# Kernel tuning notes

Hardware: AMD Instinct MI355X
Metric: run time of the kernel (lower is better)

## Reference

```python
import jax, jax.numpy as jnp
import numpy as np

N_NODES = 50000
N_EDGES = 800000
NUM_GRAPHS = 4
IN_DIM, HID_DIM, OUT_DIM = 1024, 128, 1
MAX_RISK = 5.0


def gcn_conv(x, W, b, src, dst, n):
    """PyG GCNConv: add self-loops, sym-normalize, gather-GEMM-scatter."""
    loop = jnp.arange(n, dtype=src.dtype)
    s = jnp.concatenate([src, loop])
    d = jnp.concatenate([dst, loop])
    deg = jax.ops.segment_sum(jnp.ones_like(d, dtype=x.dtype), d, num_segments=n)
    dinv = jnp.where(deg > 0, jax.lax.rsqrt(deg), 0.0)
    norm = dinv[s] * dinv[d]  # [E+N]
    xw = x @ W                # dense GEMM first (fewer FLOPs than per-edge)
    msg = xw[s] * norm[:, None]          # irregular gather, [E+N, out]
    out = jax.ops.segment_sum(msg, d, num_segments=n)  # scatter-add
    return out + b


def setup_inputs() -> dict:
    key = jax.random.key(0)
    ks = jax.random.split(key, 12)
    x = jax.random.normal(ks[0], (N_NODES, IN_DIM), dtype=jnp.float32)
    edge_index = jax.random.randint(ks[1], (2, N_EDGES), 0, N_NODES, dtype=jnp.int64)
    batch = jnp.sort(jax.random.randint(ks[2], (N_NODES,), 0, NUM_GRAPHS, dtype=jnp.int64))

    def glorot(k, fan_in, fan_out):
        s = np.sqrt(6.0 / (fan_in + fan_out)).astype(np.float32)
        return jax.random.uniform(k, (fan_in, fan_out), jnp.float32, -s, s)

    params = {
        'W0': glorot(ks[3], IN_DIM, HID_DIM),  'b0': jnp.zeros((HID_DIM,), jnp.float32),
        'W1': glorot(ks[4], HID_DIM, HID_DIM), 'b1': jnp.zeros((HID_DIM,), jnp.float32),
        'W2': glorot(ks[5], HID_DIM, HID_DIM), 'b2': jnp.zeros((HID_DIM,), jnp.float32),
        'Wl1': glorot(ks[6], 2 * HID_DIM, HID_DIM), 'bl1': jnp.zeros((HID_DIM,), jnp.float32),
        'Wl2': glorot(ks[7], HID_DIM, HID_DIM // 2), 'bl2': jnp.zeros((HID_DIM // 2,), jnp.float32),
        'Wl3': glorot(ks[8], HID_DIM // 2, OUT_DIM), 'bl3': jnp.zeros((OUT_DIM,), jnp.float32),
    }
    return dict(x=x, edge_index=edge_index, batch=batch, **params)


def reference(x, edge_index, batch, W0, b0, W1, b1, W2, b2, Wl1, bl1, Wl2, bl2, Wl3, bl3):
    n = x.shape[0]
    src, dst = edge_index[0], edge_index[1]
    h = jax.nn.relu(gcn_conv(x, W0, b0, src, dst, n))
    h = jax.nn.relu(gcn_conv(h, W1, b1, src, dst, n))
    h = jax.nn.relu(gcn_conv(h, W2, b2, src, dst, n))
    # global max pool + global mean pool per graph
    gmax = jax.ops.segment_max(h, batch, num_segments=NUM_GRAPHS)
    gsum = jax.ops.segment_sum(h, batch, num_segments=NUM_GRAPHS)
    cnt = jax.ops.segment_sum(jnp.ones((n,), h.dtype), batch, num_segments=NUM_GRAPHS)
    gmean = gsum / jnp.maximum(cnt, 1.0)[:, None]
    g = jnp.concatenate([gmax, gmean], axis=1)  # [G, 2*hid]
    g = jax.nn.relu(g @ Wl1 + bl1)
    g = jax.nn.relu(g @ Wl2 + bl2)
    out = g @ Wl3 + bl3
    return jnp.minimum(out, MAX_RISK)
```

## Files before the change

kernel.cpp:

```cpp
#include <hip/hip_runtime.h>
#include <math.h>

#define HID 128
#define NGRAPH 4

typedef int idx_t;
typedef short bf16x8 __attribute__((ext_vector_type(8)));
typedef float f32x4 __attribute__((ext_vector_type(4)));
typedef _Float16 f16x8 __attribute__((ext_vector_type(8)));

__device__ inline ushort f2bf(float f) {
  uint u = __float_as_uint(f);
  u += 0x7FFF + ((u >> 16) & 1);
  return (ushort)(u >> 16);
}
__device__ inline float bf2f(ushort h) { return __uint_as_float(((uint)h) << 16); }

__device__ inline int sw(int row, int slot) {
  return (row << 5) + ((slot ^ ((row >> 1) & 3)) << 3);
}

__global__ __launch_bounds__(256) void k_count(const idx_t* __restrict__ dst,
                                               int* __restrict__ cnt, int E) {
  int e = blockIdx.x * 256 + threadIdx.x;
  if (e < E) atomicAdd(&cnt[dst[e]], 1);
}

#define SC 1024
__global__ __launch_bounds__(256) void k_scan1(const int* __restrict__ cnt,
                                               int* __restrict__ bsum, int n) {
  __shared__ int sh[256];
  int base = blockIdx.x * SC + threadIdx.x * 4;
  int s = 0;
#pragma unroll
  for (int j = 0; j < 4; ++j) { int i = base + j; if (i < n) s += cnt[i]; }
  sh[threadIdx.x] = s;
  __syncthreads();
  for (int o = 128; o > 0; o >>= 1) {
    if (threadIdx.x < o) sh[threadIdx.x] += sh[threadIdx.x + o];
    __syncthreads();
  }
  if (threadIdx.x == 0) bsum[blockIdx.x] = sh[0];
}

__global__ __launch_bounds__(64) void k_scan2(const int* __restrict__ bsum,
                                              int* __restrict__ boff,
                                              int* __restrict__ off, int nb, int n) {
  int lane = threadIdx.x;
  int v = (lane < nb) ? bsum[lane] : 0;
  for (int d = 1; d < 64; d <<= 1) {
    int t = __shfl_up(v, d);
    if (lane >= d) v += t;
  }
  int ex = __shfl_up(v, 1);
  if (lane == 0) ex = 0;
  if (lane < nb) boff[lane] = ex;
  if (lane == nb - 1) off[n] = v;
}

__global__ __launch_bounds__(256) void k_scan3(const int* __restrict__ cnt,
                                               const int* __restrict__ boff,
                                               int* __restrict__ off,
                                               float* __restrict__ dinv, int n) {
  __shared__ int sh[256];
  int base = blockIdx.x * SC + threadIdx.x * 4;
  int c[4];
  int s = 0;
#pragma unroll
  for (int j = 0; j < 4; ++j) {
    int i = base + j;
    c[j] = (i < n) ? cnt[i] : 0;
    s += c[j];
  }
  sh[threadIdx.x] = s;
  __syncthreads();
  for (int o = 1; o < 256; o <<= 1) {
    int t = (threadIdx.x >= (unsigned)o) ? sh[threadIdx.x - o] : 0;
    __syncthreads();
    sh[threadIdx.x] += t;
    __syncthreads();
  }
  int ex = sh[threadIdx.x] - s + boff[blockIdx.x];
#pragma unroll
  for (int j = 0; j < 4; ++j) {
    int i = base + j;
    if (i < n) {
      off[i] = ex;
      dinv[i] = 1.0f / sqrtf((float)c[j] + 1.0f);
      ex += c[j];
    }
  }
}

__global__ __launch_bounds__(256) void k_fill(const idx_t* __restrict__ src,
                                              const idx_t* __restrict__ dst,
                                              const int* __restrict__ off,
                                              const float* __restrict__ dinv,
                                              int* __restrict__ fillc,
                                              int2* __restrict__ edata, int E) {
  int e = blockIdx.x * 256 + threadIdx.x;
  if (e < E) {
    int s = src[e], d = dst[e];
    int p = atomicAdd(&fillc[d], 1);
    float w = dinv[s] * dinv[d];
    edata[off[d] + p] = make_int2(s, __float_as_int(w));
  }
}

__global__ __launch_bounds__(256) void k_wsplit(const float* __restrict__ W,
                                                ushort* __restrict__ Wh,
                                                ushort* __restrict__ Wl, int K) {
  int i = blockIdx.x * 256 + threadIdx.x;
  if (i >= K * HID) return;
  int k = i >> 7, n = i & 127;
  float f = W[i];
  ushort h = f2bf(f);
  Wh[(size_t)n * K + k] = h;
  Wl[(size_t)n * K + k] = f2bf(f - bf2f(h));
}

template <int K>
__global__ __launch_bounds__(256) void k_gemm_mfma(const float* __restrict__ X,
                                                   const ushort* __restrict__ Wh,
                                                   const ushort* __restrict__ Wl,
                                                   float* __restrict__ Y,
                                                   _Float16* __restrict__ Y16,
                                                   int M) {
  __shared__ __align__(16) ushort Ah[128 * 32];
  __shared__ __align__(16) ushort Al[128 * 32];
  __shared__ __align__(16) ushort Bh[128 * 32];
  __shared__ __align__(16) ushort Bl[128 * 32];
  int tid = threadIdx.x;
  int wid = tid >> 6, lane = tid & 63;
  int lrow = lane & 15, kg = lane >> 4;
  int row0 = blockIdx.x * 128;
  f32x4 acc[2][8] = {};

  for (int k0 = 0; k0 < K; k0 += 32) {
#pragma unroll
    for (int p = 0; p < 2; ++p) {
      int g = tid + (p << 8);
      int r = g >> 2, s = g & 3;
      int grow = row0 + r;
      float xv[8] = {0.f, 0.f, 0.f, 0.f, 0.f, 0.f, 0.f, 0.f};
      if (grow < M) {
        const float4 v0 = *(const float4*)&X[(size_t)grow * K + k0 + s * 8];
        const float4 v1 = *(const float4*)&X[(size_t)grow * K + k0 + s * 8 + 4];
        xv[0] = v0.x; xv[1] = v0.y; xv[2] = v0.z; xv[3] = v0.w;
        xv[4] = v1.x; xv[5] = v1.y; xv[6] = v1.z; xv[7] = v1.w;
      }
      bf16x8 hv, lv;
#pragma unroll
      for (int j = 0; j < 8; ++j) {
        ushort hb = f2bf(xv[j]);
        hv[j] = (short)hb;
        lv[j] = (short)f2bf(xv[j] - bf2f(hb));
      }
      *(bf16x8*)&Ah[sw(r, s)] = hv;
      *(bf16x8*)&Al[sw(r, s)] = lv;
    }
#pragma unroll
    for (int p = 0; p < 2; ++p) {
      int g = tid + (p << 8);
      int c = g >> 2, s = g & 3;
      *(bf16x8*)&Bh[sw(c, s)] = *(const bf16x8*)&Wh[(size_t)c * K + k0 + s * 8];
      *(bf16x8*)&Bl[sw(c, s)] = *(const bf16x8*)&Wl[(size_t)c * K + k0 + s * 8];
    }
    __syncthreads();

    bf16x8 ah[2], al[2];
#pragma unroll
    for (int mi = 0; mi < 2; ++mi) {
      int r = wid * 32 + mi * 16 + lrow;
      ah[mi] = *(const bf16x8*)&Ah[sw(r, kg)];
      al[mi] = *(const bf16x8*)&Al[sw(r, kg)];
    }
#pragma unroll
    for (int ni = 0; ni < 8; ++ni) {
      int c = ni * 16 + lrow;
      bf16x8 bh = *(const bf16x8*)&Bh[sw(c, kg)];
      bf16x8 bl = *(const bf16x8*)&Bl[sw(c, kg)];
#pragma unroll
      for (int mi = 0; mi < 2; ++mi) {
        acc[mi][ni] = __builtin_amdgcn_mfma_f32_16x16x32_bf16(ah[mi], bh, acc[mi][ni], 0, 0, 0);
        acc[mi][ni] = __builtin_amdgcn_mfma_f32_16x16x32_bf16(al[mi], bh, acc[mi][ni], 0, 0, 0);
        acc[mi][ni] = __builtin_amdgcn_mfma_f32_16x16x32_bf16(ah[mi], bl, acc[mi][ni], 0, 0, 0);
      }
    }
    __syncthreads();
  }
#pragma unroll
  for (int mi = 0; mi < 2; ++mi)
#pragma unroll
    for (int ni = 0; ni < 8; ++ni)
#pragma unroll
      for (int r = 0; r < 4; ++r) {
        int grow = row0 + wid * 32 + mi * 16 + kg * 4 + r;
        if (grow < M) {
          float val = acc[mi][ni][r];
          Y[(size_t)grow * HID + ni * 16 + lrow] = val;
          Y16[(size_t)grow * HID + ni * 16 + lrow] = (_Float16)val;
        }
      }
}

__global__ __launch_bounds__(256) void k_agg16(const float* __restrict__ xw,
                                               const _Float16* __restrict__ xh,
                                               const float* __restrict__ dinv,
                                               const int* __restrict__ off,
                                               const int2* __restrict__ edata,
                                               const float* __restrict__ bias,
                                               float* __restrict__ hout, int n) {
  int v = blockIdx.x * 4 + (threadIdx.x >> 6);
  if (v >= n) return;
  int lane = threadIdx.x & 63;
  int grp = lane >> 4, gl = lane & 15;
  int fb = gl * 8;
  float acc[8] = {0.f, 0.f, 0.f, 0.f, 0.f, 0.f, 0.f, 0.f};
  int j0 = off[v], j1 = off[v + 1];
  for (int j = j0 + grp; j < j1; j += 4) {
    int2 e = edata[j];
    float w = __int_as_float(e.y);
    f16x8 m = *(const f16x8*)&xh[(size_t)e.x * HID + fb];
#pragma unroll
    for (int q = 0; q < 8; ++q) acc[q] = fmaf(w, (float)m[q], acc[q]);
  }
#pragma unroll
  for (int q = 0; q < 8; ++q) {
    acc[q] += __shfl_xor(acc[q], 16);
    acc[q] += __shfl_xor(acc[q], 32);
  }
  if (grp == 0) {
    float dv = dinv[v], dv2 = dv * dv;
    const float4 s0 = *(const float4*)&xw[(size_t)v * HID + fb];
    const float4 s1 = *(const float4*)&xw[(size_t)v * HID + fb + 4];
    const float4 b0 = *(const float4*)&bias[fb];
    const float4 b1 = *(const float4*)&bias[fb + 4];
    float4 o0, o1;
    o0.x = fmaxf(fmaf(dv2, s0.x, acc[0]) + b0.x, 0.f);
    o0.y = fmaxf(fmaf(dv2, s0.y, acc[1]) + b0.y, 0.f);
    o0.z = fmaxf(fmaf(dv2, s0.z, acc[2]) + b0.z, 0.f);
    o0.w = fmaxf(fmaf(dv2, s0.w, acc[3]) + b0.w, 0.f);
    o1.x = fmaxf(fmaf(dv2, s1.x, acc[4]) + b1.x, 0.f);
    o1.y = fmaxf(fmaf(dv2, s1.y, acc[5]) + b1.y, 0.f);
    o1.z = fmaxf(fmaf(dv2, s1.z, acc[6]) + b1.z, 0.f);
    o1.w = fmaxf(fmaf(dv2, s1.w, acc[7]) + b1.w, 0.f);
    *(float4*)&hout[(size_t)v * HID + fb] = o0;
    *(float4*)&hout[(size_t)v * HID + fb + 4] = o1;
  }
}

__global__ __launch_bounds__(256) void k_gcnt(const idx_t* __restrict__ batch,
                                              int* __restrict__ gcnt, int n) {
  __shared__ int h[NGRAPH];
  int tid = threadIdx.x;
  if (tid < NGRAPH) h[tid] = 0;
  __syncthreads();
  int i = blockIdx.x * 256 + tid;
  if (i < n) atomicAdd(&h[batch[i]], 1);
  __syncthreads();
  if (tid < NGRAPH && h[tid]) atomicAdd(&gcnt[tid], h[tid]);
}

__global__ __launch_bounds__(128) void k_pool(const float* __restrict__ h,
                                              const idx_t* __restrict__ batch,
                                              float* __restrict__ gmax,
                                              float* __restrict__ gsum, int n) {
  int f = threadIdx.x;
  int v0 = blockIdx.x * 128;
  int cur = -1;
  float mx = 0.f, sm = 0.f;
  for (int i = 0; i < 128; ++i) {
    int v = v0 + i;
    if (v >= n) break;
    int g = batch[v];
    if (g != cur) {
      if (cur >= 0) {
        atomicMax((int*)&gmax[cur * HID + f], __float_as_int(mx));
        atomicAdd(&gsum[cur * HID + f], sm);
      }
      cur = g; mx = 0.f; sm = 0.f;
    }
    float val = h[(size_t)v * HID + f];
    mx = fmaxf(mx, val);
    sm += val;
  }
  if (cur >= 0) {
    atomicMax((int*)&gmax[cur * HID + f], __float_as_int(mx));
    atomicAdd(&gsum[cur * HID + f], sm);
  }
}

__global__ __launch_bounds__(256) void k_mlp(const float* __restrict__ gmax,
                                             const float* __restrict__ gsum,
                                             const int* __restrict__ gcnt,
                                             const float* __restrict__ Wl1,
                                             const float* __restrict__ bl1,
                                             const float* __restrict__ Wl2,
                                             const float* __restrict__ bl2,
                                             const float* __restrict__ Wl3,
                                             const float* __restrict__ bl3,
                                             float* __restrict__ out) {
  __shared__ float G[NGRAPH][2 * HID];
  __shared__ float H1[NGRAPH][HID];
  __shared__ float H2[NGRAPH][HID / 2];
  int t = threadIdx.x;
  for (int i = t; i < NGRAPH * 2 * HID; i += 256) {
    int gi = i >> 8, j = i & 255;
    float val;
    if (j < HID) val = gmax[gi * HID + j];
    else val = gsum[gi * HID + (j - HID)] / fmaxf((float)gcnt[gi], 1.0f);
    G[gi][j] = val;
  }
  __syncthreads();
  for (int i = t; i < NGRAPH * HID; i += 256) {
    int gi = i >> 7, j = i & 127;
    float a = bl1[j];
    for (int k = 0; k < 2 * HID; ++k) a = fmaf(G[gi][k], Wl1[k * HID + j], a);
    H1[gi][j] = fmaxf(a, 0.f);
  }
  __syncthreads();
  {
    int gi = t >> 6, j = t & 63;
    float a = bl2[j];
    for (int k = 0; k < HID; ++k) a = fmaf(H1[gi][k], Wl2[k * 64 + j], a);
    H2[gi][j] = fmaxf(a, 0.f);
  }
  __syncthreads();
  if (t < NGRAPH) {
    float a = bl3[0];
    for (int k = 0; k < 64; ++k) a = fmaf(H2[t][k], Wl3[k], a);
    out[t] = fminf(a, 5.0f);
  }
}

extern "C" void kernel_launch(void* const* d_in, const int* in_sizes, int n_in,
                              void* d_out, int out_size, void* d_ws, size_t ws_size,
                              hipStream_t stream) {
  const float* x   = (const float*)d_in[0];
  const idx_t* ei  = (const idx_t*)d_in[1];
  const idx_t* bat = (const idx_t*)d_in[2];
  const float* W0 = (const float*)d_in[3];  const float* b0 = (const float*)d_in[4];
  const float* W1 = (const float*)d_in[5];  const float* b1 = (const float*)d_in[6];
  const float* W2 = (const float*)d_in[7];  const float* b2 = (const float*)d_in[8];
  const float* Wl1 = (const float*)d_in[9];  const float* bl1 = (const float*)d_in[10];
  const float* Wl2 = (const float*)d_in[11]; const float* bl2 = (const float*)d_in[12];
  const float* Wl3 = (const float*)d_in[13]; const float* bl3 = (const float*)d_in[14];
  float* out = (float*)d_out;

  const int N = in_sizes[2];
  const int E = in_sizes[1] / 2;
  const idx_t* srcv = ei;
  const idx_t* dstv = ei + E;
  const int nb = (N + SC - 1) / SC;

  char* ws = (char*)d_ws;
  size_t o = 0;
  auto alloc = [&](size_t bytes) -> void* {
    void* p = ws + o;
    o = (o + bytes + 255) & ~(size_t)255;
    return p;
  };
  float* bufA      = (float*)alloc((size_t)N * HID * 4);
  _Float16* bufA16 = (_Float16*)alloc((size_t)N * HID * 2);
  float* bufB      = (float*)alloc((size_t)N * HID * 4);
  float* dinv = (float*)alloc((size_t)N * 4);
  int* cnt    = (int*)alloc((size_t)N * 4);
  int* off    = (int*)alloc((size_t)(N + 1) * 4);
  int* fillc  = (int*)alloc((size_t)N * 4);
  int2* edata = (int2*)alloc((size_t)E * 8);
  int* bsum   = (int*)alloc(64 * 4);
  int* boff   = (int*)alloc(64 * 4);
  ushort* Wh0 = (ushort*)alloc((size_t)1024 * HID * 2);
  ushort* Wl0 = (ushort*)alloc((size_t)1024 * HID * 2);
  ushort* Wh1 = (ushort*)alloc((size_t)HID * HID * 2);
  ushort* Wlo1 = (ushort*)alloc((size_t)HID * HID * 2);
  ushort* Wh2 = (ushort*)alloc((size_t)HID * HID * 2);
  ushort* Wlo2 = (ushort*)alloc((size_t)HID * HID * 2);
  float* gmax = (float*)alloc(NGRAPH * HID * 4);
  float* gsum = (float*)alloc(NGRAPH * HID * 4);
  int* gcnt   = (int*)alloc(NGRAPH * 4);

  hipMemsetAsync(cnt, 0, (size_t)N * 4, stream);
  hipMemsetAsync(fillc, 0, (size_t)N * 4, stream);
  hipMemsetAsync(gmax, 0, NGRAPH * HID * 4, stream);
  hipMemsetAsync(gsum, 0, NGRAPH * HID * 4, stream);
  hipMemsetAsync(gcnt, 0, NGRAPH * 4, stream);

  k_wsplit<<<(1024 * HID + 255) / 256, 256, 0, stream>>>(W0, Wh0, Wl0, 1024);
  k_wsplit<<<(HID * HID + 255) / 256, 256, 0, stream>>>(W1, Wh1, Wlo1, HID);
  k_wsplit<<<(HID * HID + 255) / 256, 256, 0, stream>>>(W2, Wh2, Wlo2, HID);

  k_count<<<(E + 255) / 256, 256, 0, stream>>>(dstv, cnt, E);
  k_scan1<<<nb, 256, 0, stream>>>(cnt, bsum, N);
  k_scan2<<<1, 64, 0, stream>>>(bsum, boff, off, nb, N);
  k_scan3<<<nb, 256, 0, stream>>>(cnt, boff, off, dinv, N);
  k_fill<<<(E + 255) / 256, 256, 0, stream>>>(srcv, dstv, off, dinv, fillc, edata, E);

  const int gblk = (N + 127) / 128;
  const int ablk = (N + 3) / 4;
  k_gemm_mfma<1024><<<gblk, 256, 0, stream>>>(x, Wh0, Wl0, bufA, bufA16, N);
  k_agg16<<<ablk, 256, 0, stream>>>(bufA, bufA16, dinv, off, edata, b0, bufB, N);
  k_gemm_mfma<HID><<<gblk, 256, 0, stream>>>(bufB, Wh1, Wlo1, bufA, bufA16, N);
  k_agg16<<<ablk, 256, 0, stream>>>(bufA, bufA16, dinv, off, edata, b1, bufB, N);
  k_gemm_mfma<HID><<<gblk, 256, 0, stream>>>(bufB, Wh2, Wlo2, bufA, bufA16, N);
  k_agg16<<<ablk, 256, 0, stream>>>(bufA, bufA16, dinv, off, edata, b2, bufB, N);

  k_gcnt<<<(N + 255) / 256, 256, 0, stream>>>(bat, gcnt, N);
  k_pool<<<(N + 127) / 128, 128, 0, stream>>>(bufB, bat, gmax, gsum, N);
  k_mlp<<<1, 256, 0, stream>>>(gmax, gsum, gcnt, Wl1, bl1, Wl2, bl2, Wl3, bl3, out);
}
```

Measured before the change: 410.0 us.

## Split-K the first GEMM and drop the fp32 GEMM output copy

The 1024-wide first-layer GEMM is split four ways along K across a second grid dimension. Each split writes fp32 partials, and a new reduction kernel sums them into fp16. This gives 1564 blocks instead of 391 to fill the GPU's CUs. The GEMMs also stop writing the fp32 copy, and aggregation reads its self-loop term from the fp16 buffer, which removes a store and a read of N*128 floats per layer. In exchange, split-K adds 4x N*128 fp32 partial writes plus a reduction pass, and the self-loop term loses precision.

```diff
diff --git a/kernel.cpp b/kernel.cpp
--- a/kernel.cpp
+++ b/kernel.cpp
@@ -119,11 +119,11 @@
   Wl[(size_t)n * K + k] = f2bf(f - bf2f(h));
 }
 
-template <int K>
+template <int K, int KS>
 __global__ __launch_bounds__(256) void k_gemm_mfma(const float* __restrict__ X,
                                                    const ushort* __restrict__ Wh,
                                                    const ushort* __restrict__ Wl,
-                                                   float* __restrict__ Y,
+                                                   float* __restrict__ Ypart,
                                                    _Float16* __restrict__ Y16,
                                                    int M) {
   __shared__ __align__(16) ushort Ah[128 * 32];
@@ -134,9 +134,11 @@
   int wid = tid >> 6, lane = tid & 63;
   int lrow = lane & 15, kg = lane >> 4;
   int row0 = blockIdx.x * 128;
+  constexpr int KC = K / KS;
+  int kbase = (KS > 1) ? blockIdx.y * KC : 0;
   f32x4 acc[2][8] = {};
 
-  for (int k0 = 0; k0 < K; k0 += 32) {
+  for (int k0 = kbase; k0 < kbase + KC; k0 += 32) {
 #pragma unroll
     for (int p = 0; p < 2; ++p) {
       int g = tid + (p << 8);
@@ -189,23 +191,49 @@
     }
     __syncthreads();
   }
-#pragma unroll
-  for (int mi = 0; mi < 2; ++mi)
-#pragma unroll
-    for (int ni = 0; ni < 8; ++ni)
-#pragma unroll
-      for (int r = 0; r < 4; ++r) {
-        int grow = row0 + wid * 32 + mi * 16 + kg * 4 + r;
-        if (grow < M) {
-          float val = acc[mi][ni][r];
-          Y[(size_t)grow * HID + ni * 16 + lrow] = val;
-          Y16[(size_t)grow * HID + ni * 16 + lrow] = (_Float16)val;
+  if (KS > 1) {
+    float* yp = Ypart + (size_t)blockIdx.y * M * HID;
+#pragma unroll
+    for (int mi = 0; mi < 2; ++mi)
+#pragma unroll
+      for (int ni = 0; ni < 8; ++ni)
+#pragma unroll
+        for (int r = 0; r < 4; ++r) {
+          int grow = row0 + wid * 32 + mi * 16 + kg * 4 + r;
+          if (grow < M) yp[(size_t)grow * HID + ni * 16 + lrow] = acc[mi][ni][r];
         }
-      }
-}
-
-__global__ __launch_bounds__(256) void k_agg16(const float* __restrict__ xw,
-                                               const _Float16* __restrict__ xh,
+  } else {
+#pragma unroll
+    for (int mi = 0; mi < 2; ++mi)
+#pragma unroll
+      for (int ni = 0; ni < 8; ++ni)
+#pragma unroll
+        for (int r = 0; r < 4; ++r) {
+          int grow = row0 + wid * 32 + mi * 16 + kg * 4 + r;
+          if (grow < M)
+            Y16[(size_t)grow * HID + ni * 16 + lrow] = (_Float16)acc[mi][ni][r];
+        }
+  }
+}
+
+__global__ __launch_bounds__(256) void k_red(const float* __restrict__ part,
+                                             _Float16* __restrict__ o16,
+                                             size_t total) {
+  size_t i = ((size_t)blockIdx.x * 256 + threadIdx.x) * 4;
+  if (i >= total) return;
+  float4 a = *(const float4*)&part[i];
+  float4 b = *(const float4*)&part[i + total];
+  float4 c = *(const float4*)&part[i + 2 * total];
+  float4 d = *(const float4*)&part[i + 3 * total];
+  _Float16 r[4];
+  r[0] = (_Float16)(a.x + b.x + c.x + d.x);
+  r[1] = (_Float16)(a.y + b.y + c.y + d.y);
+  r[2] = (_Float16)(a.z + b.z + c.z + d.z);
+  r[3] = (_Float16)(a.w + b.w + c.w + d.w);
+  *(short4*)&o16[i] = *(short4*)r;
+}
+
+__global__ __launch_bounds__(256) void k_agg16(const _Float16* __restrict__ xh,
                                                const float* __restrict__ dinv,
                                                const int* __restrict__ off,
                                                const int2* __restrict__ edata,
@@ -232,19 +260,18 @@
   }
   if (grp == 0) {
     float dv = dinv[v], dv2 = dv * dv;
-    const float4 s0 = *(const float4*)&xw[(size_t)v * HID + fb];
-    const float4 s1 = *(const float4*)&xw[(size_t)v * HID + fb + 4];
+    f16x8 sv = *(const f16x8*)&xh[(size_t)v * HID + fb];
     const float4 b0 = *(const float4*)&bias[fb];
     const float4 b1 = *(const float4*)&bias[fb + 4];
     float4 o0, o1;
-    o0.x = fmaxf(fmaf(dv2, s0.x, acc[0]) + b0.x, 0.f);
-    o0.y = fmaxf(fmaf(dv2, s0.y, acc[1]) + b0.y, 0.f);
-    o0.z = fmaxf(fmaf(dv2, s0.z, acc[2]) + b0.z, 0.f);
-    o0.w = fmaxf(fmaf(dv2, s0.w, acc[3]) + b0.w, 0.f);
-    o1.x = fmaxf(fmaf(dv2, s1.x, acc[4]) + b1.x, 0.f);
-    o1.y = fmaxf(fmaf(dv2, s1.y, acc[5]) + b1.y, 0.f);
-    o1.z = fmaxf(fmaf(dv2, s1.z, acc[6]) + b1.z, 0.f);
-    o1.w = fmaxf(fmaf(dv2, s1.w, acc[7]) + b1.w, 0.f);
+    o0.x = fmaxf(fmaf(dv2, (float)sv[0], acc[0]) + b0.x, 0.f);
+    o0.y = fmaxf(fmaf(dv2, (float)sv[1], acc[1]) + b0.y, 0.f);
+    o0.z = fmaxf(fmaf(dv2, (float)sv[2], acc[2]) + b0.z, 0.f);
+    o0.w = fmaxf(fmaf(dv2, (float)sv[3], acc[3]) + b0.w, 0.f);
+    o1.x = fmaxf(fmaf(dv2, (float)sv[4], acc[4]) + b1.x, 0.f);
+    o1.y = fmaxf(fmaf(dv2, (float)sv[5], acc[5]) + b1.y, 0.f);
+    o1.z = fmaxf(fmaf(dv2, (float)sv[6], acc[6]) + b1.z, 0.f);
+    o1.w = fmaxf(fmaf(dv2, (float)sv[7], acc[7]) + b1.w, 0.f);
     *(float4*)&hout[(size_t)v * HID + fb] = o0;
     *(float4*)&hout[(size_t)v * HID + fb + 4] = o1;
   }
@@ -361,9 +388,9 @@
     o = (o + bytes + 255) & ~(size_t)255;
     return p;
   };
-  float* bufA      = (float*)alloc((size_t)N * HID * 4);
-  _Float16* bufA16 = (_Float16*)alloc((size_t)N * HID * 2);
-  float* bufB      = (float*)alloc((size_t)N * HID * 4);
+  _Float16* xh   = (_Float16*)alloc((size_t)N * HID * 2);
+  float* bufB    = (float*)alloc((size_t)N * HID * 4);
+  float* part    = (float*)alloc((size_t)4 * N * HID * 4);
   float* dinv = (float*)alloc((size_t)N * 4);
   int* cnt    = (int*)alloc((size_t)N * 4);
   int* off    = (int*)alloc((size_t)(N + 1) * 4);
@@ -399,12 +426,14 @@
 
   const int gblk = (N + 127) / 128;
   const int ablk = (N + 3) / 4;
-  k_gemm_mfma<1024><<<gblk, 256, 0, stream>>>(x, Wh0, Wl0, bufA, bufA16, N);
-  k_agg16<<<ablk, 256, 0, stream>>>(bufA, bufA16, dinv, off, edata, b0, bufB, N);
-  k_gemm_mfma<HID><<<gblk, 256, 0, stream>>>(bufB, Wh1, Wlo1, bufA, bufA16, N);
-  k_agg16<<<ablk, 256, 0, stream>>>(bufA, bufA16, dinv, off, edata, b1, bufB, N);
-  k_gemm_mfma<HID><<<gblk, 256, 0, stream>>>(bufB, Wh2, Wlo2, bufA, bufA16, N);
-  k_agg16<<<ablk, 256, 0, stream>>>(bufA, bufA16, dinv, off, edata, b2, bufB, N);
+  const size_t total = (size_t)N * HID;
+  k_gemm_mfma<1024, 4><<<dim3(gblk, 4), 256, 0, stream>>>(x, Wh0, Wl0, part, nullptr, N);
+  k_red<<<(int)((total / 4 + 255) / 256), 256, 0, stream>>>(part, xh, total);
+  k_agg16<<<ablk, 256, 0, stream>>>(xh, dinv, off, edata, b0, bufB, N);
+  k_gemm_mfma<HID, 1><<<gblk, 256, 0, stream>>>(bufB, Wh1, Wlo1, nullptr, xh, N);
+  k_agg16<<<ablk, 256, 0, stream>>>(xh, dinv, off, edata, b1, bufB, N);
+  k_gemm_mfma<HID, 1><<<gblk, 256, 0, stream>>>(bufB, Wh2, Wlo2, nullptr, xh, N);
+  k_agg16<<<ablk, 256, 0, stream>>>(xh, dinv, off, edata, b2, bufB, N);
 
   k_gcnt<<<(N + 255) / 256, 256, 0, stream>>>(bat, gcnt, N);
   k_pool<<<(N + 127) / 128, 128, 0, stream>>>(bufB, bat, gmax, gsum, N);
```

Result: slower. 431.6 us (+5.3%).
